# Optimization experiments

Measured on AMD Instinct MI355X. Metric: run time of the kernel, lower is better.

## Reference

```python
import jax, jax.numpy as jnp
import numpy as np

E = 2        # expan_att_chans
HEADS = 16   # num_chans * expan_att_chans


def _gconv1x1(x, w, b, groups):
    # Grouped 1x1 conv. x: [B, Cin, H, W]; w: [Cout, Cin//groups]; b: [Cout].
    # Output channel layout matches torch: group-major (c_group * gout + o).
    B, Cin, H, W = x.shape
    Cout = w.shape[0]
    gin, gout = Cin // groups, Cout // groups
    y = jnp.einsum('bgip,goi->bgop',
                   x.reshape(B, groups, gin, H * W),
                   w.reshape(groups, gout, gin))
    return y.reshape(B, Cout, H, W) + b[None, :, None, None]


def _l2norm(x, eps=1e-12):
    # F.normalize(dim=-1): x / max(||x||_2, eps)
    n = jnp.sqrt(jnp.sum(x * x, axis=-1, keepdims=True))
    return x / jnp.maximum(n, eps)


def setup_inputs() -> dict:
    key = jax.random.key(0)
    ks = jax.random.split(key, 12)
    B, C, H, W = 8, 128, 128, 128
    s = 0.05  # small init (module uses xavier gain=0.01)
    f32 = jnp.float32
    return {
        'x': jax.random.normal(ks[0], (B, C, H, W), f32),
        'to': jax.random.normal(ks[1], (B, C, H, W), f32),
        't': jnp.ones((1, HEADS, 1, 1), f32),
        # rgb qkv chain (fusion): C -> 2EC -> EC -> EC, all groups=C
        'w_r1': (jax.random.normal(ks[2], (C * E * 2, 1), f32) * s),
        'b_r1': jnp.zeros((C * E * 2,), f32),
        'w_r2': (jax.random.normal(ks[3], (C * E, 2 * E), f32) * s),
        'b_r2': jnp.zeros((C * E,), f32),
        'w_r3': (jax.random.normal(ks[4], (C * E, E), f32) * s),
        'b_r3': jnp.zeros((C * E,), f32),
        # text kv chain: C -> 2EC -> EC -> 2EC, all groups=C
        'w_t1': (jax.random.normal(ks[5], (C * E * 2, 1), f32) * s),
        'b_t1': jnp.zeros((C * E * 2,), f32),
        'w_t2': (jax.random.normal(ks[6], (C * E, 2 * E), f32) * s),
        'b_t2': jnp.zeros((C * E,), f32),
        'w_t3': (jax.random.normal(ks[7], (C * E * 2, E), f32) * s),
        'b_t3': jnp.zeros((C * E * 2,), f32),
        # fusion conv: Conv2d(E*C -> C, k=3, stride=1, pad=1) + LeakyReLU(0.2)
        'w_f': (jax.random.normal(ks[8], (C, C * E, 3, 3), f32) * 0.02),
        'b_f': jnp.zeros((C,), f32),
    }


def reference(x, to, t, w_r1, b_r1, w_r2, b_r2, w_r3, b_r3,
              w_t1, b_t1, w_t2, b_t2, w_t3, b_t3, w_f, b_f):
    B, C, H, W = x.shape
    Cexp = E * C
    d = Cexp // HEADS  # per-head channel dim
    HW = H * W

    # grouped 1x1 conv chains producing Q (from rgb) and K,V (from text)
    q = _gconv1x1(_gconv1x1(_gconv1x1(x, w_r1, b_r1, C), w_r2, b_r2, C), w_r3, b_r3, C)      # [B, EC, H, W]
    kv = _gconv1x1(_gconv1x1(_gconv1x1(to, w_t1, b_t1, C), w_t2, b_t2, C), w_t3, b_t3, C)    # [B, 2EC, H, W]

    # Rearrange 'B (C E) H W -> B E C H W' then view as [B, heads, d, HW]
    q = q.reshape(B, C, E, HW).transpose(0, 2, 1, 3).reshape(B, HEADS, d, HW)
    kv = kv.reshape(B, C, 2 * E, HW).transpose(0, 2, 1, 3)  # [B, 2E, C, HW]
    k = kv[:, :E].reshape(B, HEADS, d, HW)
    v = kv[:, E:].reshape(B, HEADS, d, HW)

    # channel (transposed) attention with L2-normalized Q,K and learned temperature
    qn, kn = _l2norm(q), _l2norm(k)
    attn = jax.nn.softmax(jnp.einsum('bhdp,bhep->bhde', qn, kn) * t, axis=-1)  # [B, H, d, d]
    xo = jnp.einsum('bhde,bhep->bhdp', attn, v)  # [B, heads, d, HW]

    # rearrange 'B C X (H W) -> B (X C) H W' with C=heads, X=d  (d-major, head-minor)
    xo = xo.transpose(0, 2, 1, 3).reshape(B, Cexp, H, W)

    # group_fus: 3x3 conv (stride 1, pad 1) + LeakyReLU(0.2), residual add
    y = jax.lax.conv_general_dilated(
        xo, w_f, window_strides=(1, 1), padding=((1, 1), (1, 1)),
        dimension_numbers=('NCHW', 'OIHW', 'NCHW'))
    y = jax.nn.leaky_relu(y + b_f[None, :, None, None], negative_slope=0.2)
    return x + y
```

## Files before the change

### kernel.cpp

```cpp
#include <hip/hip_runtime.h>
#include <math.h>

#define B_  8
#define C_  128
#define H_  128
#define W_  128
#define HW_ 16384

#define OFF_MPART 0
#define OFF_SPART 262144
#define OFF_M     327680
#define OFF_S     344064
#define OFF_WV    348160
#define OFF_CST   380928
#define OFF_T     382976
#define OFF_WEFF  392192
#define OFF_T2F   982016
#define T2_ROW    16640
#define T2_BATCH  2163200
#define WS_NEED   (982016ull * 4ull + 34611200ull)

typedef __attribute__((ext_vector_type(8))) short short8;
typedef __attribute__((ext_vector_type(4))) float f32x4;

__device__ __forceinline__ unsigned short f2bf(float f) {
  unsigned u = __float_as_uint(f);
  u += 0x7fffu + ((u >> 16) & 1u);
  return (unsigned short)(u >> 16);
}

__device__ __forceinline__ f32x4 mfma16(short8 a, short8 b, f32x4 c) {
  return __builtin_amdgcn_mfma_f32_16x16x32_bf16(a, b, c, 0, 0, 0);
}

__device__ __forceinline__ void gl16(const void* g, void* l) {
  const unsigned loff = (unsigned)(unsigned long long)l;
  __builtin_amdgcn_global_load_lds(
      (const __attribute__((address_space(1))) void*)g,
      (__attribute__((address_space(3))) void*)loff, 16, 0, 0);
}

__device__ __forceinline__ float wave_sum64(float v) {
  v += __shfl_xor(v, 1);
  v += __shfl_xor(v, 2);
  v += __shfl_xor(v, 4);
  v += __shfl_xor(v, 8);
  v += __shfl_xor(v, 16);
  v += __shfl_xor(v, 32);
  return v;
}

__global__ __launch_bounds__(256) void k_reduce(const float* __restrict__ x,
                                                const float* __restrict__ to,
                                                float* __restrict__ ws) {
  const int bid  = blockIdx.x;
  const int kc   = bid & 15;
  const int blk  = (bid >> 4) & 7;
  const int b    = bid >> 7;
  const int wave = threadIdx.x >> 6;
  const int lane = threadIdx.x & 63;
  const int c0   = blk * 16;
  const int i0   = wave * 4;

  const float* xb = x  + ((size_t)b * C_ + c0) * HW_;
  const float* tb = to + ((size_t)b * C_ + c0) * HW_;

  float acc[4][16];
#pragma unroll
  for (int a = 0; a < 4; ++a)
#pragma unroll
    for (int j = 0; j < 16; ++j) acc[a][j] = 0.f;
  float sx[4] = {0,0,0,0}, sxx[4] = {0,0,0,0}, st[4] = {0,0,0,0}, stt[4] = {0,0,0,0};

  const int pbase = kc * 1024 + lane;
#pragma unroll 1
  for (int it = 0; it < 16; ++it) {
    const int p = pbase + it * 64;
    float tv[16];
#pragma unroll
    for (int j = 0; j < 16; ++j) tv[j] = tb[j * HW_ + p];
    float xv[4];
#pragma unroll
    for (int a = 0; a < 4; ++a) xv[a] = xb[(i0 + a) * HW_ + p];
#pragma unroll
    for (int a = 0; a < 4; ++a)
#pragma unroll
      for (int j = 0; j < 16; ++j) acc[a][j] = fmaf(xv[a], tv[j], acc[a][j]);
#pragma unroll
    for (int a = 0; a < 4; ++a) { sx[a] += xv[a]; sxx[a] = fmaf(xv[a], xv[a], sxx[a]); }
#pragma unroll
    for (int j = 0; j < 16; ++j)
      if ((j >> 2) == wave) { st[j & 3] += tv[j]; stt[j & 3] = fmaf(tv[j], tv[j], stt[j & 3]); }
  }

#pragma unroll
  for (int a = 0; a < 4; ++a) {
#pragma unroll
    for (int j = 0; j < 16; ++j) acc[a][j] = wave_sum64(acc[a][j]);
    sx[a]  = wave_sum64(sx[a]);
    sxx[a] = wave_sum64(sxx[a]);
    st[a]  = wave_sum64(st[a]);
    stt[a] = wave_sum64(stt[a]);
  }

  if (lane == 0) {
    float* Mp = ws + OFF_MPART + (size_t)((b * 8 + blk) * 16 + kc) * 256;
#pragma unroll
    for (int a = 0; a < 4; ++a)
#pragma unroll
      for (int j = 0; j < 16; ++j) Mp[(i0 + a) * 16 + j] = acc[a][j];
    float* Sp = ws + OFF_SPART;
#pragma unroll
    for (int a = 0; a < 4; ++a) {
      const int cidx = b * C_ + c0 + i0 + a;
      Sp[0 * 16384 + cidx * 16 + kc] = sx[a];
      Sp[1 * 16384 + cidx * 16 + kc] = sxx[a];
      Sp[2 * 16384 + cidx * 16 + kc] = st[a];
      Sp[3 * 16384 + cidx * 16 + kc] = stt[a];
    }
  }
}

__global__ __launch_bounds__(256) void k_redB(float* __restrict__ ws) {
  const int gid = blockIdx.x * 256 + threadIdx.x;
  if (gid < 16384) {
    const float* mp = ws + OFF_MPART + (size_t)(gid >> 8) * 4096 + (gid & 255);
    float s = 0.f;
#pragma unroll
    for (int kc = 0; kc < 16; ++kc) s += mp[kc * 256];
    ws[OFF_M + gid] = s;
  } else {
    const int sidx = gid - 16384;
    const float* sp = ws + OFF_SPART + (size_t)sidx * 16;
    float s = 0.f;
#pragma unroll
    for (int kc = 0; kc < 16; ++kc) s += sp[kc];
    ws[OFF_S + sidx] = s;
  }
}

__global__ __launch_bounds__(256) void k_zero(unsigned short* __restrict__ t2) {
  const int b = blockIdx.x >> 1, r = blockIdx.x & 1;
  unsigned short* row = t2 + (size_t)b * T2_BATCH + (size_t)(r ? 129 : 0) * T2_ROW;
  const short8 z = {0,0,0,0,0,0,0,0};
  for (int idx = threadIdx.x; idx < 2080; idx += 256)
    *(short8*)(row + (size_t)idx * 8) = z;
}

__global__ __launch_bounds__(256) void k_tr(const float* __restrict__ to,
                                            unsigned short* __restrict__ t2) {
  const int d  = blockIdx.x;
  const int xh = d & 1;
  const int y  = (d >> 1) & 127;
  const int b  = d >> 8;
  const int tid = threadIdx.x;
  __shared__ char lds[64 * 256];

  const int x0 = xh * 64;
  const int xl = tid & 63;
  const int cg = tid >> 6;
  const float* src = to + ((size_t)b * C_) * HW_ + (size_t)y * W_ + x0 + xl;
#pragma unroll
  for (int k = 0; k < 32; ++k) {
    const int c = cg * 32 + k;
    const float v = src[(size_t)c * HW_];
    const int boff = xl * 256 + ((2 * c) ^ ((xl & 7) << 4));
    *(unsigned short*)(lds + boff) = f2bf(v);
  }
  __syncthreads();

  unsigned short* rowbase = t2 + (size_t)b * T2_BATCH + (size_t)(y + 1) * T2_ROW;
#pragma unroll
  for (int i = 0; i < 4; ++i) {
    const int xx = tid >> 2;
    const int cs = (tid & 3) + i * 4;
    short8 val = *(short8*)(lds + xx * 256 + ((cs * 16) ^ ((xx & 7) << 4)));
    *(short8*)(rowbase + (size_t)(x0 + xx + 1) * 128 + cs * 8) = val;
  }
  if (tid < 16) {
    short8 z = {0,0,0,0,0,0,0,0};
    if (xh == 0) *(short8*)(rowbase + tid * 8) = z;
    else         *(short8*)(rowbase + (size_t)129 * 128 + tid * 8) = z;
  }
}

__global__ __launch_bounds__(256) void k_attn(const float* __restrict__ t,
    const float* __restrict__ w_r1, const float* __restrict__ b_r1,
    const float* __restrict__ w_r2, const float* __restrict__ b_r2,
    const float* __restrict__ w_r3, const float* __restrict__ b_r3,
    const float* __restrict__ w_t1, const float* __restrict__ b_t1,
    const float* __restrict__ w_t2, const float* __restrict__ b_t2,
    const float* __restrict__ w_t3, const float* __restrict__ b_t3,
    float* __restrict__ ws) {
  const int b = blockIdx.x;
  const int tid = threadIdx.x;
  __shared__ float aQ[256], bQ[256], aK[256], bK[256], aV[256], bV[256];
  __shared__ float rks[256], kAs[256], kBs[256], stos[256];

  if (tid < 128) {
    const int g = tid;
    float A1[4], B1[4], A2[2], B2[2];
#pragma unroll
    for (int j = 0; j < 4; ++j) { A1[j] = w_r1[g * 4 + j]; B1[j] = b_r1[g * 4 + j]; }
#pragma unroll
    for (int i = 0; i < 2; ++i) {
      A2[i] = 0.f; B2[i] = b_r2[g * 2 + i];
#pragma unroll
      for (int j = 0; j < 4; ++j) {
        const float w = w_r2[(g * 2 + i) * 4 + j];
        A2[i] = fmaf(w, A1[j], A2[i]); B2[i] = fmaf(w, B1[j], B2[i]);
      }
    }
#pragma unroll
    for (int o = 0; o < 2; ++o) {
      float a = 0.f, bb = b_r3[g * 2 + o];
#pragma unroll
      for (int i = 0; i < 2; ++i) {
        const float w = w_r3[(g * 2 + o) * 2 + i];
        a = fmaf(w, A2[i], a); bb = fmaf(w, B2[i], bb);
      }
      aQ[g * 2 + o] = a; bQ[g * 2 + o] = bb;
    }
#pragma unroll
    for (int j = 0; j < 4; ++j) { A1[j] = w_t1[g * 4 + j]; B1[j] = b_t1[g * 4 + j]; }
#pragma unroll
    for (int i = 0; i < 2; ++i) {
      A2[i] = 0.f; B2[i] = b_t2[g * 2 + i];
#pragma unroll
      for (int j = 0; j < 4; ++j) {
        const float w = w_t2[(g * 2 + i) * 4 + j];
        A2[i] = fmaf(w, A1[j], A2[i]); B2[i] = fmaf(w, B1[j], B2[i]);
      }
    }
#pragma unroll
    for (int o = 0; o < 4; ++o) {
      float a = 0.f, bb = b_t3[g * 4 + o];
#pragma unroll
      for (int i = 0; i < 2; ++i) {
        const float w = w_t3[(g * 4 + o) * 2 + i];
        a = fmaf(w, A2[i], a); bb = fmaf(w, B2[i], bb);
      }
      if (o < 2) { aK[g * 2 + o] = a; bK[g * 2 + o] = bb; }
      else       { aV[g * 2 + (o - 2)] = a; bV[g * 2 + (o - 2)] = bb; }
    }
  }
  __syncthreads();

  const float* S   = ws + OFF_S;
  const float* Sx  = S;
  const float* Sxx = S + 1024;
  const float* Sto = S + 2048;
  const float* Stt = S + 3072;

  {
    const int h = tid >> 4, e = h >> 3, blk = h & 7, c0 = blk * 16;
    const int g = c0 + (tid & 15);
    const float a = aK[g * 2 + e], bb = bK[g * 2 + e];
    const float s2 = a * a * Stt[b * C_ + g] + 2.f * a * bb * Sto[b * C_ + g]
                   + bb * bb * 16384.f;
    rks[tid] = 1.f / fmaxf(sqrtf(fmaxf(s2, 0.f)), 1e-12f);
    kAs[tid] = a; kBs[tid] = bb;
    stos[tid] = Sto[b * C_ + g];
  }
  __syncthreads();

  {
    const int h = tid >> 4, i = tid & 15, e = h >> 3, blk = h & 7, c0 = blk * 16;
    const int gi = c0 + i;
    const float gA = aQ[gi * 2 + e], gB = bQ[gi * 2 + e];
    const float sxi = Sx[b * C_ + gi];
    const float q2 = gA * gA * Sxx[b * C_ + gi] + 2.f * gA * gB * sxi
                   + gB * gB * 16384.f;
    const float rnq = 1.f / fmaxf(sqrtf(fmaxf(q2, 0.f)), 1e-12f);
    const float tt = t[h];
    const float* Mrow = ws + OFF_M + (size_t)(b * 8 + blk) * 256 + i * 16;

    float lg[16];
    float mx = -1e30f;
#pragma unroll
    for (int j = 0; j < 16; ++j) {
      const float s = gA * kAs[h * 16 + j] * Mrow[j]
                    + gA * kBs[h * 16 + j] * sxi
                    + gB * kAs[h * 16 + j] * stos[h * 16 + j]
                    + gB * kBs[h * 16 + j] * 16384.f;
      const float l = tt * s * rnq * rks[h * 16 + j];
      lg[j] = l;
      mx = fmaxf(mx, l);
    }
    float den = 0.f;
#pragma unroll
    for (int j = 0; j < 16; ++j) { const float ev = expf(lg[j] - mx); lg[j] = ev; den += ev; }
    const float inv = 1.f / den;
    float cs = 0.f;
    float* WVp = ws + OFF_WV + (size_t)(b * 16 + h) * 256 + i * 16;
#pragma unroll
    for (int j = 0; j < 16; ++j) {
      const float aa = lg[j] * inv;
      const int gj = c0 + j;
      WVp[j] = aa * aV[gj * 2 + e];
      cs = fmaf(aa, bV[gj * 2 + e], cs);
    }
    ws[OFF_CST + b * 256 + i * 16 + h] = cs;
  }
}

__global__ __launch_bounds__(128) void k_weff(const float* __restrict__ w_f,
                                              float* __restrict__ ws) {
  const int b = blockIdx.x >> 7, oc = blockIdx.x & 127;
  const int c = threadIdx.x, blk = c >> 4, j = c & 15;
  const float* WVb = ws + OFF_WV;
  float acc[9];
#pragma unroll
  for (int k = 0; k < 9; ++k) acc[k] = 0.f;
#pragma unroll
  for (int e = 0; e < 2; ++e) {
    const int h = e * 8 + blk;
#pragma unroll
    for (int i = 0; i < 16; ++i) {
      const float coef = WVb[((size_t)(b * 16 + h) * 16 + i) * 16 + j];
      const float* wf = w_f + (size_t)(oc * 256 + i * 16 + h) * 9;
#pragma unroll
      for (int k = 0; k < 9; ++k) acc[k] = fmaf(wf[k], coef, acc[k]);
    }
  }
  unsigned short* wb16 = (unsigned short*)(ws + OFF_WEFF);
#pragma unroll
  for (int k = 0; k < 9; ++k)
    wb16[(((size_t)(b * 9 + k)) * 128 + oc) * 128 + c] = f2bf(acc[k]);

  __shared__ float tp[9][128];
  float tl[9];
#pragma unroll
  for (int k = 0; k < 9; ++k) tl[k] = 0.f;
  const float* cst = ws + OFF_CST + b * 256;
  for (int cc = c; cc < 256; cc += 128) {
    const float cv = cst[cc];
    const float* wf = w_f + (size_t)(oc * 256 + cc) * 9;
#pragma unroll
    for (int k = 0; k < 9; ++k) tl[k] = fmaf(wf[k], cv, tl[k]);
  }
#pragma unroll
  for (int k = 0; k < 9; ++k) tp[k][c] = tl[k];
  __syncthreads();
  for (int s = 64; s > 0; s >>= 1) {
    if (c < s) {
#pragma unroll
      for (int k = 0; k < 9; ++k) tp[k][c] += tp[k][c + s];
    }
    __syncthreads();
  }
  if (c < 9) ws[OFF_T + ((size_t)b * 128 + oc) * 9 + c] = tp[c][0];
}

__global__ __launch_bounds__(512, 4) void k_conv(const float* __restrict__ xin,
                                                 const float* __restrict__ b_f,
                                                 const float* __restrict__ ws,
                                                 const unsigned short* __restrict__ t2,
                                                 float* __restrict__ out) {
  const int d = blockIdx.x;
  const int b = d & 7;
  const int y = d >> 3;
  const int tid = threadIdx.x;

  __shared__ unsigned short As[2][128 * 64];
  __shared__ unsigned short Bs[2][128 * 64];

  const unsigned short* wb = (const unsigned short*)(ws + OFF_WEFF)
      + (size_t)b * 9 * 16384;
  const unsigned short* t2y = t2 + (size_t)b * T2_BATCH + (size_t)y * T2_ROW;

  const int l = tid & 63;
  const int lm = l & 15, lh = l >> 4;
  const int wv = tid >> 6;
  const int oc0w = (wv >> 1) * 32;
  const int px0w = (wv & 1) * 64;

  const int trow0 = tid >> 3, tci0 = tid & 7;
  const unsigned udst0 = (unsigned)((tid & ~63) * 16);
  const unsigned udst1 = udst0 + 512u * 16u;

#define STAGE(BUF, S)                                                          \
  {                                                                            \
    const int tap_ = (S) >> 1, ks_ = (S) & 1;                                  \
    const int dy_ = tap_ / 3, dx_ = tap_ - dy_ * 3;                            \
    const unsigned short* asrc = wb + (size_t)tap_ * 16384 + ks_ * 64;         \
    const unsigned short* bsrc = t2y + (size_t)dy_ * T2_ROW + dx_ * 128 + ks_ * 64; \
    gl16(asrc + (size_t)trow0 * 128 + ((tci0 ^ (trow0 & 7)) << 3),             \
         (char*)&As[BUF][0] + udst0);                                          \
    gl16(asrc + (size_t)(trow0 + 64) * 128 + ((tci0 ^ ((trow0 + 64) & 7)) << 3), \
         (char*)&As[BUF][0] + udst1);                                          \
    gl16(bsrc + (size_t)trow0 * 128 + ((tci0 ^ (trow0 & 7)) << 3),             \
         (char*)&Bs[BUF][0] + udst0);                                          \
    gl16(bsrc + (size_t)(trow0 + 64) * 128 + ((tci0 ^ ((trow0 + 64) & 7)) << 3), \
         (char*)&Bs[BUF][0] + udst1);                                          \
  }

  f32x4 acc[2][4];
#pragma unroll
  for (int mt = 0; mt < 2; ++mt)
#pragma unroll
    for (int nt = 0; nt < 4; ++nt) acc[mt][nt] = (f32x4)0.f;

  STAGE(0, 0);
  __syncthreads();

  int cur = 0;
#pragma unroll 1
  for (int s = 0; s < 18; ++s) {
    if (s + 1 < 18) STAGE(cur ^ 1, s + 1);

    const char* Ab = (const char*)&As[cur][0];
    const char* Bb = (const char*)&Bs[cur][0];
#pragma unroll
    for (int ki = 0; ki < 2; ++ki) {
      short8 af[2], bfr[4];
#pragma unroll
      for (int mt = 0; mt < 2; ++mt) {
        const int oc = oc0w + mt * 16 + lm;
        af[mt] = *(const short8*)(Ab + oc * 128 + (((ki * 4 + lh) ^ (oc & 7)) << 4));
      }
#pragma unroll
      for (int nt = 0; nt < 4; ++nt) {
        const int px = px0w + nt * 16 + lm;
        bfr[nt] = *(const short8*)(Bb + px * 128 + (((ki * 4 + lh) ^ (px & 7)) << 4));
      }
#pragma unroll
      for (int mt = 0; mt < 2; ++mt) {
        acc[mt][0] = mfma16(af[mt], bfr[0], acc[mt][0]);
        acc[mt][1] = mfma16(af[mt], bfr[1], acc[mt][1]);
        acc[mt][2] = mfma16(af[mt], bfr[2], acc[mt][2]);
        acc[mt][3] = mfma16(af[mt], bfr[3], acc[mt][3]);
      }
    }
    __syncthreads();
    cur ^= 1;
  }
#undef STAGE

  float* sm = (float*)&As[0][0];
  if (tid < 128) {
    const float* Tk = ws + OFF_T + (size_t)(b * 128 + tid) * 9;
    float s = Tk[3] + Tk[4] + Tk[5], sl = Tk[3], sr = Tk[5];
    if (y >= 1)   { s += Tk[0] + Tk[1] + Tk[2]; sl += Tk[0]; sr += Tk[2]; }
    if (y <= 126) { s += Tk[6] + Tk[7] + Tk[8]; sl += Tk[6]; sr += Tk[8]; }
    sm[tid] = s + b_f[tid]; sm[128 + tid] = sl; sm[256 + tid] = sr;
  }
  __syncthreads();

#pragma unroll
  for (int mt = 0; mt < 2; ++mt)
#pragma unroll
    for (int nt = 0; nt < 4; ++nt) {
      const int px = px0w + nt * 16 + lm;
#pragma unroll
      for (int r = 0; r < 4; ++r) {
        const int oc = oc0w + mt * 16 + lh * 4 + r;
        float add = sm[oc];
        if (px == 0)   add -= sm[128 + oc];
        if (px == 127) add -= sm[256 + oc];
        const float z = acc[mt][nt][r] + add;
        const size_t base = ((size_t)(b * C_ + oc)) * HW_ + (size_t)y * W_ + px;
        const float rx = xin[base];
        out[base] = rx + (z >= 0.f ? z : 0.2f * z);
      }
    }
}

__global__ __launch_bounds__(512, 4) void k_conv_fb(const float* __restrict__ xin,
                                                    const float* __restrict__ to,
                                                    const float* __restrict__ b_f,
                                                    const float* __restrict__ ws,
                                                    float* __restrict__ out) {
  const int bid = blockIdx.x;
  const int nb  = (bid & 7) * 128 + (bid >> 3);
  const int b   = nb >> 7;
  const int y   = nb & 127;
  const int tid = threadIdx.x;

  __shared__ f32x4 ldsbuf[3120];
  char* lp = (char*)ldsbuf;

  f32x4 acc[4][2];
#pragma unroll
  for (int mt = 0; mt < 4; ++mt)
#pragma unroll
    for (int nt = 0; nt < 2; ++nt) acc[mt][nt] = (f32x4)0.f;

  const float* tob = to + (size_t)b * C_ * HW_;
  const unsigned short* wb16 =
      (const unsigned short*)(ws + OFF_WEFF) + (size_t)b * 9 * 128 * 128;

  const int l = tid & 63, wv = tid >> 6;
  const int ocb0 = (wv & 1) * 64, pxb0 = (wv >> 1) * 32;
  const int lm = l & 15, lh = l >> 4;

  for (int cb = 0; cb < 128; cb += 64) {
    __syncthreads();
    {
      const int xg = tid & 31, cq = (tid >> 5) & 15;
      const int cbase = cb + cq * 4;
#pragma unroll
      for (int row = 0; row < 3; ++row) {
        const int y_in = y + row - 1;
        const bool yok = ((unsigned)y_in < 128u);
        const float* src = tob + (size_t)cbase * HW_ + (size_t)y_in * W_;
#pragma unroll
        for (int xb = 0; xb < 5; ++xb) {
          const int xi = xb * 32 + xg;
          if (xi < 130) {
            const int x_in = xi - 1;
            const bool ok = yok && ((unsigned)x_in < 128u);
            float f0 = 0.f, f1 = 0.f, f2 = 0.f, f3 = 0.f;
            if (ok) {
              f0 = src[x_in];
              f1 = src[HW_ + x_in];
              f2 = src[2 * HW_ + x_in];
              f3 = src[3 * HW_ + x_in];
            }
            ushort4 pk;
            pk.x = f2bf(f0); pk.y = f2bf(f1); pk.z = f2bf(f2); pk.w = f2bf(f3);
            const int boff = (row * 130 + xi) * 128 + ((cq * 8) ^ ((xi & 7) << 4));
            *(ushort4*)(lp + boff) = pk;
          }
        }
      }
    }
    __syncthreads();

    for (int tap = 0; tap < 9; ++tap) {
      const int dy = tap / 3, dx = tap - dy * 3;
#pragma unroll
      for (int ks = 0; ks < 2; ++ks) {
        short8 bfr[2];
#pragma unroll
        for (int nt = 0; nt < 2; ++nt) {
          const int xi = pxb0 + nt * 16 + lm + dx;
          const int boff = (dy * 130 + xi) * 128 + ((ks * 64 + lh * 16) ^ ((xi & 7) << 4));
          bfr[nt] = *(const short8*)(lp + boff);
        }
        const int cin = cb + ks * 32 + lh * 8;
#pragma unroll
        for (int mt = 0; mt < 4; ++mt) {
          const int oc = ocb0 + mt * 16 + lm;
          const short8 af = *(const short8*)(wb16 + ((size_t)tap * 128 + oc) * 128 + cin);
          acc[mt][0] = mfma16(af, bfr[0], acc[mt][0]);
          acc[mt][1] = mfma16(af, bfr[1], acc[mt][1]);
        }
      }
    }
  }

  __syncthreads();
  float* sAdd = (float*)ldsbuf;
  float* sLft = sAdd + 128;
  float* sRgt = sAdd + 256;
  if (tid < 128) {
    const float* Tk = ws + OFF_T + (size_t)(b * 128 + tid) * 9;
    float s = Tk[3] + Tk[4] + Tk[5], sl = Tk[3], sr = Tk[5];
    if (y >= 1)   { s += Tk[0] + Tk[1] + Tk[2]; sl += Tk[0]; sr += Tk[2]; }
    if (y <= 126) { s += Tk[6] + Tk[7] + Tk[8]; sl += Tk[6]; sr += Tk[8]; }
    sAdd[tid] = s + b_f[tid]; sLft[tid] = sl; sRgt[tid] = sr;
  }
  __syncthreads();

#pragma unroll
  for (int mt = 0; mt < 4; ++mt)
#pragma unroll
    for (int nt = 0; nt < 2; ++nt) {
      const int px = pxb0 + nt * 16 + lm;
#pragma unroll
      for (int r = 0; r < 4; ++r) {
        const int oc = ocb0 + mt * 16 + lh * 4 + r;
        float add = sAdd[oc];
        if (px == 0)   add -= sLft[oc];
        if (px == 127) add -= sRgt[oc];
        const float z = acc[mt][nt][r] + add;
        const size_t base = ((size_t)(b * C_ + oc)) * HW_ + (size_t)y * W_ + px;
        const float rx = xin[base];
        out[base] = rx + (z >= 0.f ? z : 0.2f * z);
      }
    }
}

extern "C" void kernel_launch(void* const* d_in, const int* in_sizes, int n_in,
                              void* d_out, int out_size, void* d_ws, size_t ws_size,
                              hipStream_t stream) {
  (void)in_sizes; (void)n_in; (void)out_size;
  const float* x    = (const float*)d_in[0];
  const float* to   = (const float*)d_in[1];
  const float* t    = (const float*)d_in[2];
  const float* w_r1 = (const float*)d_in[3];
  const float* b_r1 = (const float*)d_in[4];
  const float* w_r2 = (const float*)d_in[5];
  const float* b_r2 = (const float*)d_in[6];
  const float* w_r3 = (const float*)d_in[7];
  const float* b_r3 = (const float*)d_in[8];
  const float* w_t1 = (const float*)d_in[9];
  const float* b_t1 = (const float*)d_in[10];
  const float* w_t2 = (const float*)d_in[11];
  const float* b_t2 = (const float*)d_in[12];
  const float* w_t3 = (const float*)d_in[13];
  const float* b_t3 = (const float*)d_in[14];
  const float* w_f  = (const float*)d_in[15];
  const float* b_f  = (const float*)d_in[16];
  float* ws  = (float*)d_ws;
  float* out = (float*)d_out;
  unsigned short* t2 = (unsigned short*)(ws + OFF_T2F);
  const bool fast = (ws_size >= WS_NEED);

  k_reduce<<<1024, 256, 0, stream>>>(x, to, ws);
  k_redB<<<80, 256, 0, stream>>>(ws);
  if (fast) {
    k_zero<<<16, 256, 0, stream>>>(t2);
    k_tr<<<2048, 256, 0, stream>>>(to, t2);
  }
  k_attn<<<8, 256, 0, stream>>>(t, w_r1, b_r1, w_r2, b_r2, w_r3, b_r3,
                                w_t1, b_t1, w_t2, b_t2, w_t3, b_t3, ws);
  k_weff<<<1024, 128, 0, stream>>>(w_f, ws);
  if (fast) k_conv<<<1024, 512, 0, stream>>>(x, b_f, ws, t2, out);
  else      k_conv_fb<<<1024, 512, 0, stream>>>(x, to, b_f, ws, out);
}
```

Baseline: 128.9 us.

## Compute x·to Gram partials with bf16 MFMA and vectorize transpose loads

```diff
diff --git a/kernel.cpp b/kernel.cpp
--- a/kernel.cpp
+++ b/kernel.cpp
@@ -40,84 +40,72 @@
       (__attribute__((address_space(3))) void*)loff, 16, 0, 0);
 }
 
-__device__ __forceinline__ float wave_sum64(float v) {
-  v += __shfl_xor(v, 1);
-  v += __shfl_xor(v, 2);
-  v += __shfl_xor(v, 4);
-  v += __shfl_xor(v, 8);
-  v += __shfl_xor(v, 16);
-  v += __shfl_xor(v, 32);
-  return v;
-}
-
-__global__ __launch_bounds__(256) void k_reduce(const float* __restrict__ x,
-                                                const float* __restrict__ to,
-                                                float* __restrict__ ws) {
-  const int bid  = blockIdx.x;
-  const int kc   = bid & 15;
-  const int blk  = (bid >> 4) & 7;
-  const int b    = bid >> 7;
-  const int wave = threadIdx.x >> 6;
-  const int lane = threadIdx.x & 63;
-  const int c0   = blk * 16;
-  const int i0   = wave * 4;
-
-  const float* xb = x  + ((size_t)b * C_ + c0) * HW_;
-  const float* tb = to + ((size_t)b * C_ + c0) * HW_;
-
-  float acc[4][16];
-#pragma unroll
-  for (int a = 0; a < 4; ++a)
-#pragma unroll
-    for (int j = 0; j < 16; ++j) acc[a][j] = 0.f;
-  float sx[4] = {0,0,0,0}, sxx[4] = {0,0,0,0}, st[4] = {0,0,0,0}, stt[4] = {0,0,0,0};
-
-  const int pbase = kc * 1024 + lane;
-#pragma unroll 1
-  for (int it = 0; it < 16; ++it) {
-    const int p = pbase + it * 64;
-    float tv[16];
-#pragma unroll
-    for (int j = 0; j < 16; ++j) tv[j] = tb[j * HW_ + p];
-    float xv[4];
-#pragma unroll
-    for (int a = 0; a < 4; ++a) xv[a] = xb[(i0 + a) * HW_ + p];
-#pragma unroll
-    for (int a = 0; a < 4; ++a)
-#pragma unroll
-      for (int j = 0; j < 16; ++j) acc[a][j] = fmaf(xv[a], tv[j], acc[a][j]);
-#pragma unroll
-    for (int a = 0; a < 4; ++a) { sx[a] += xv[a]; sxx[a] = fmaf(xv[a], xv[a], sxx[a]); }
-#pragma unroll
-    for (int j = 0; j < 16; ++j)
-      if ((j >> 2) == wave) { st[j & 3] += tv[j]; stt[j & 3] = fmaf(tv[j], tv[j], stt[j & 3]); }
-  }
-
-#pragma unroll
-  for (int a = 0; a < 4; ++a) {
-#pragma unroll
-    for (int j = 0; j < 16; ++j) acc[a][j] = wave_sum64(acc[a][j]);
-    sx[a]  = wave_sum64(sx[a]);
-    sxx[a] = wave_sum64(sxx[a]);
-    st[a]  = wave_sum64(st[a]);
-    stt[a] = wave_sum64(stt[a]);
-  }
-
-  if (lane == 0) {
-    float* Mp = ws + OFF_MPART + (size_t)((b * 8 + blk) * 16 + kc) * 256;
-#pragma unroll
-    for (int a = 0; a < 4; ++a)
-#pragma unroll
-      for (int j = 0; j < 16; ++j) Mp[(i0 + a) * 16 + j] = acc[a][j];
-    float* Sp = ws + OFF_SPART;
-#pragma unroll
-    for (int a = 0; a < 4; ++a) {
-      const int cidx = b * C_ + c0 + i0 + a;
-      Sp[0 * 16384 + cidx * 16 + kc] = sx[a];
-      Sp[1 * 16384 + cidx * 16 + kc] = sxx[a];
-      Sp[2 * 16384 + cidx * 16 + kc] = st[a];
-      Sp[3 * 16384 + cidx * 16 + kc] = stt[a];
-    }
+__global__ __launch_bounds__(256) void k_gram(const float* __restrict__ x,
+                                              const float* __restrict__ to,
+                                              float* __restrict__ ws) {
+  const int bid = blockIdx.x;
+  const int ps  = bid & 15;
+  const int blk = (bid >> 4) & 7;
+  const int b   = bid >> 7;
+  const int tid = threadIdx.x;
+  const int w = tid >> 6, l = tid & 63;
+  const int lm = l & 15, lh = l >> 4;
+  const int c0 = blk * 16;
+
+  const float* xc = x  + ((size_t)b * C_ + c0 + lm) * HW_;
+  const float* tc = to + ((size_t)b * C_ + c0 + lm) * HW_;
+  const int p0 = ps * 1024 + w * 256 + lh * 8;
+
+  f32x4 acc = (f32x4)0.f;
+  float sx = 0.f, sxx = 0.f, st = 0.f, stt = 0.f;
+#pragma unroll
+  for (int it = 0; it < 8; ++it) {
+    const int p = p0 + it * 32;
+    const f32x4 xa = *(const f32x4*)(xc + p);
+    const f32x4 xb = *(const f32x4*)(xc + p + 4);
+    const f32x4 ta = *(const f32x4*)(tc + p);
+    const f32x4 tb = *(const f32x4*)(tc + p + 4);
+    short8 xf, tf;
+#pragma unroll
+    for (int e = 0; e < 4; ++e) {
+      xf[e]     = (short)f2bf(xa[e]);
+      xf[4 + e] = (short)f2bf(xb[e]);
+      tf[e]     = (short)f2bf(ta[e]);
+      tf[4 + e] = (short)f2bf(tb[e]);
+      sx += xa[e] + xb[e];
+      sxx = fmaf(xa[e], xa[e], fmaf(xb[e], xb[e], sxx));
+      st += ta[e] + tb[e];
+      stt = fmaf(ta[e], ta[e], fmaf(tb[e], tb[e], stt));
+    }
+    acc = mfma16(xf, tf, acc);
+  }
+
+  sx  += __shfl_xor(sx, 16);  sx  += __shfl_xor(sx, 32);
+  sxx += __shfl_xor(sxx, 16); sxx += __shfl_xor(sxx, 32);
+  st  += __shfl_xor(st, 16);  st  += __shfl_xor(st, 32);
+  stt += __shfl_xor(stt, 16); stt += __shfl_xor(stt, 32);
+
+  __shared__ float smM[4][256];
+  __shared__ float smS[4][4][16];
+#pragma unroll
+  for (int r = 0; r < 4; ++r)
+    smM[w][(lh * 4 + r) * 16 + lm] = acc[r];
+  if (l < 16) {
+    smS[w][0][lm] = sx;  smS[w][1][lm] = sxx;
+    smS[w][2][lm] = st;  smS[w][3][lm] = stt;
+  }
+  __syncthreads();
+
+  {
+    const float s = smM[0][tid & 255] + smM[1][tid & 255]
+                  + smM[2][tid & 255] + smM[3][tid & 255];
+    ws[OFF_MPART + (size_t)((b * 8 + blk) * 16 + ps) * 256 + tid] = s;
+  }
+  if (tid < 64) {
+    const int kind = tid >> 4, ch = tid & 15;
+    const float s = smS[0][kind][ch] + smS[1][kind][ch]
+                  + smS[2][kind][ch] + smS[3][kind][ch];
+    ws[OFF_SPART + (size_t)kind * 16384 + (size_t)(b * C_ + c0 + ch) * 16 + ps] = s;
   }
 }
 
@@ -157,15 +145,19 @@
   __shared__ char lds[64 * 256];
 
   const int x0 = xh * 64;
-  const int xl = tid & 63;
-  const int cg = tid >> 6;
-  const float* src = to + ((size_t)b * C_) * HW_ + (size_t)y * W_ + x0 + xl;
-#pragma unroll
-  for (int k = 0; k < 32; ++k) {
-    const int c = cg * 32 + k;
-    const float v = src[(size_t)c * HW_];
-    const int boff = xl * 256 + ((2 * c) ^ ((xl & 7) << 4));
-    *(unsigned short*)(lds + boff) = f2bf(v);
+  const int xq = tid & 15;
+  const int cg = tid >> 4;
+  const float* srcb = to + ((size_t)b * C_ + cg * 8) * HW_ + (size_t)y * W_ + x0 + xq * 4;
+#pragma unroll
+  for (int k = 0; k < 8; ++k) {
+    const f32x4 v = *(const f32x4*)(srcb + (size_t)k * HW_);
+    const int c = cg * 8 + k;
+#pragma unroll
+    for (int e = 0; e < 4; ++e) {
+      const int xl = xq * 4 + e;
+      const int boff = xl * 256 + ((2 * c) ^ ((xl & 7) << 4));
+      *(unsigned short*)(lds + boff) = f2bf(v[e]);
+    }
   }
   __syncthreads();
 
@@ -608,7 +600,7 @@
   unsigned short* t2 = (unsigned short*)(ws + OFF_T2F);
   const bool fast = (ws_size >= WS_NEED);
 
-  k_reduce<<<1024, 256, 0, stream>>>(x, to, ws);
+  k_gram<<<1024, 256, 0, stream>>>(x, to, ws);
   k_redB<<<80, 256, 0, stream>>>(ws);
   if (fast) {
     k_zero<<<16, 256, 0, stream>>>(t2);
```

Measured after the change: 113.1 us. 12.3% less time.
